# Optimization experiments

Hardware: AMD Instinct MI355X
Metric: run time of the kernel (lower is better)

Reference implementation:

```python
import jax, jax.numpy as jnp
import numpy as np

N_NODES = 100000
N_EDGES = 1600000
N_GRAPHS = 1000
IN_C = 64
HID = 64
OUT_C = 1
L = 3


def setup_inputs() -> dict:
    key = jax.random.key(0)
    ks = jax.random.split(key, 12)
    x = jax.random.normal(ks[0], (N_NODES, IN_C), dtype=jnp.float32)
    edge_index = jax.random.randint(ks[1], (2, N_EDGES), 0, N_NODES, dtype=jnp.int32)
    batch = jnp.sort(jax.random.randint(ks[2], (N_NODES,), 0, N_GRAPHS, dtype=jnp.int32))
    s = 1.0 / np.sqrt(HID)
    # GraphConv params (all layers 64->64): lin_rel (W,b) applied to aggregated
    # neighbors, lin_root (W, no bias) applied to self features.
    Wrel = jax.random.uniform(ks[3], (L, HID, HID), jnp.float32, -s, s)
    brel = jax.random.uniform(ks[4], (L, HID), jnp.float32, -s, s)
    Wroot = jax.random.uniform(ks[5], (L, HID, HID), jnp.float32, -s, s)
    W1 = jax.random.uniform(ks[6], (HID, 64), jnp.float32, -s, s)
    b1 = jax.random.uniform(ks[7], (64,), jnp.float32, -s, s)
    W2 = jax.random.uniform(ks[8], (64, 32), jnp.float32, -1/8, 1/8)
    b2 = jax.random.uniform(ks[9], (32,), jnp.float32, -1/8, 1/8)
    W3 = jax.random.uniform(ks[10], (32, OUT_C), jnp.float32, -1/np.sqrt(32), 1/np.sqrt(32))
    b3 = jax.random.uniform(ks[11], (OUT_C,), jnp.float32, -1/np.sqrt(32), 1/np.sqrt(32))
    return {"x": x, "edge_index": edge_index, "batch": batch,
            "Wrel": Wrel, "brel": brel, "Wroot": Wroot,
            "W1": W1, "b1": b1, "W2": W2, "b2": b2, "W3": W3, "b3": b3}


def reference(x, edge_index, batch, Wrel, brel, Wroot, W1, b1, W2, b2, W3, b3):
    src, dst = edge_index[0], edge_index[1]
    n = x.shape[0]
    x_add = jnp.zeros((N_GRAPHS, HID), dtype=x.dtype)
    for i in range(L):
        # GraphConv: gather source features, sum-scatter to targets
        agg = jax.ops.segment_sum(x[src], dst, num_segments=n)  # [N, C]
        x = agg @ Wrel[i] + brel[i] + x @ Wroot[i]
        x = jax.nn.relu(x)
        # global_add_pool per layer, accumulated
        x_add = x_add + jax.ops.segment_sum(x, batch, num_segments=N_GRAPHS)
    h = jax.nn.relu(x_add @ W1 + b1)
    h = jax.nn.relu(h @ W2 + b2)
    return h @ W3 + b3  # [N_GRAPHS, OUT_C]
```

## Files before the change

kernel.cpp:

```cpp
#include <hip/hip_runtime.h>
#include <hip/hip_bf16.h>

#define HID 64
#define BN 192
#define MAXB 1024

typedef short  bf16x8 __attribute__((ext_vector_type(8)));
typedef float  f32x4  __attribute__((ext_vector_type(4)));

__device__ inline float bf2f(unsigned int u16) {
    union { unsigned int i; float f; } v; v.i = u16 << 16; return v.f;
}
__device__ inline unsigned short f2bf(float f) {
    union { float f; unsigned int i; } v; v.f = f;
    unsigned int u = v.i;
    u += 0x7FFFu + ((u >> 16) & 1u);
    return (unsigned short)(u >> 16);
}

__global__ __launch_bounds__(1024) void bucket_hist(
        const int* __restrict__ dst, int* __restrict__ cnt, int E, int nb) {
    __shared__ int h[MAXB];
    for (int i = threadIdx.x; i < nb; i += 1024) h[i] = 0;
    __syncthreads();
    int base = blockIdx.x * 16384;
    for (int i = 0; i < 16; ++i) {
        int e = base + i * 1024 + threadIdx.x;
        if (e < E) atomicAdd(&h[dst[e] / BN], 1);
    }
    __syncthreads();
    for (int i = threadIdx.x; i < nb; i += 1024)
        if (h[i]) atomicAdd(&cnt[i], h[i]);
}

__global__ void bucket_scan(const int* __restrict__ cnt, int* __restrict__ base,
                            int* __restrict__ cursor, int nb, int total) {
    int lane = threadIdx.x;
    int running = 0;
    int nch = (nb + 63) / 64;
    for (int c = 0; c < nch; ++c) {
        int i = c * 64 + lane;
        int v = (i < nb) ? cnt[i] : 0;
        int s = v;
        for (int d = 1; d < 64; d <<= 1) {
            int t = __shfl_up(s, d);
            if (lane >= d) s += t;
        }
        if (i < nb) {
            int ex = running + s - v;
            base[i] = ex;
            cursor[i * 16] = ex;
        }
        running += __shfl(s, 63);
    }
    if (lane == 0) base[nb] = total;
}

__global__ __launch_bounds__(1024) void bucket_scatter(
        const int* __restrict__ src, const int* __restrict__ dst,
        int* __restrict__ cursor, unsigned int* __restrict__ rec, int E, int nb) {
    __shared__ int h[MAXB];
    __shared__ int gb[MAXB];
    __shared__ int lc[MAXB];
    for (int i = threadIdx.x; i < nb; i += 1024) { h[i] = 0; lc[i] = 0; }
    __syncthreads();
    int base = blockIdx.x * 16384;
    for (int i = 0; i < 16; ++i) {
        int e = base + i * 1024 + threadIdx.x;
        if (e < E) atomicAdd(&h[dst[e] / BN], 1);
    }
    __syncthreads();
    for (int i = threadIdx.x; i < nb; i += 1024) {
        int c = h[i];
        if (c) gb[i] = atomicAdd(&cursor[i * 16], c);
    }
    __syncthreads();
    for (int i = 0; i < 16; ++i) {
        int e = base + i * 1024 + threadIdx.x;
        if (e < E) {
            int d = dst[e];
            int b = d / BN;
            int lp = atomicAdd(&lc[b], 1);
            rec[gb[b] + lp] = ((unsigned int)src[e] << 8) | (unsigned int)(d - b * BN);
        }
    }
}

__global__ __launch_bounds__(256) void bucket_to_csr(
        const unsigned int* __restrict__ rec, const int* __restrict__ bbase,
        int* __restrict__ col, int* __restrict__ rowp, int N, int nb) {
    __shared__ int tmp[256];
    __shared__ int cur[256];
    int b = blockIdx.x;
    int n0 = b * BN;
    int nNodes = min(BN, N - n0);
    int tid = threadIdx.x;
    int e0 = bbase[b], e1 = bbase[b + 1];
    tmp[tid] = 0;
    __syncthreads();
    for (int e = e0 + tid; e < e1; e += 256)
        atomicAdd(&tmp[rec[e] & 255u], 1);
    __syncthreads();
    int my = tmp[tid];
    for (int offd = 1; offd < 256; offd <<= 1) {
        int t = (tid >= offd) ? tmp[tid - offd] : 0;
        __syncthreads();
        tmp[tid] += t;
        __syncthreads();
    }
    int ex = tmp[tid] - my;
    cur[tid] = ex;
    if (tid < nNodes) rowp[n0 + tid] = e0 + ex;
    if (b == nb - 1 && tid == 0) rowp[N] = e1;
    __syncthreads();
    for (int e = e0 + tid; e < e1; e += 256) {
        unsigned int r = rec[e];
        int p = atomicAdd(&cur[r & 255u], 1);
        col[e0 + p] = (int)(r >> 8);
    }
}

__global__ __launch_bounds__(256) void prep_all(
        const float* __restrict__ x0, unsigned int* __restrict__ xb,
        const float* __restrict__ Wrel, const float* __restrict__ Wroot,
        unsigned short* __restrict__ Wt,
        const int* __restrict__ batch, int* __restrict__ bstart,
        int* __restrict__ bcnt, float* __restrict__ x_add,
        int N, int G, int nl, int NB) {
    int i = blockIdx.x * 256 + threadIdx.x;
    if (i < N * 16) {
        float4 v = reinterpret_cast<const float4*>(x0)[i];
        xb[i * 2]     = ((unsigned int)f2bf(v.y) << 16) | f2bf(v.x);
        xb[i * 2 + 1] = ((unsigned int)f2bf(v.w) << 16) | f2bf(v.z);
    }
    if (i < nl * 64 * 128) {
        int k = i & 127, c = (i >> 7) & 63, l = i >> 13;
        float v = (k < 64) ? Wrel[(size_t)l * 4096 + k * 64 + c]
                           : Wroot[(size_t)l * 4096 + (k - 64) * 64 + c];
        Wt[i] = f2bf(v);
    }
    if (i < N) {
        int b = batch[i];
        int prev = (i == 0) ? -1 : batch[i - 1];
        for (int g = prev + 1; g <= b; ++g) bstart[g] = i;
        if (i == N - 1)
            for (int g = b + 1; g <= G; ++g) bstart[g] = N;
    }
    if (i < NB) bcnt[i] = 0;
    if (i < G * 64) x_add[i] = 0.f;
}

__global__ __launch_bounds__(256) void layer_fused(
        const int* __restrict__ rowp, const int* __restrict__ col,
        const unsigned int* __restrict__ xb,
        unsigned short* __restrict__ yout,
        const unsigned short* __restrict__ Wt,
        const float* __restrict__ brel, int n) {
    __shared__ unsigned int aggL[16][36];
    int n0 = blockIdx.x * 16;
    int tid = threadIdx.x;
    int lane = tid & 63;
    int wv = tid >> 6;
    int half = lane >> 5, ch = lane & 31;

#pragma unroll
    for (int s = 0; s < 2; ++s) {
        int node = n0 + wv * 4 + half * 2 + s;
        if (node < n) {
            int e0 = rowp[node], e1 = rowp[node + 1];
            float ax = 0.f, ay = 0.f;
            for (int eb = e0; eb < e1; eb += 8) {
                int c[8];
#pragma unroll
                for (int j = 0; j < 8; ++j) c[j] = col[min(eb + j, e1 - 1)];
                unsigned int p[8];
#pragma unroll
                for (int j = 0; j < 8; ++j) p[j] = xb[(size_t)c[j] * 32 + ch];
#pragma unroll
                for (int j = 0; j < 8; ++j) {
                    unsigned int q = (eb + j < e1) ? p[j] : 0u;
                    ax += bf2f(q & 0xFFFFu);
                    ay += bf2f(q >> 16);
                }
            }
            aggL[node - n0][ch] = ((unsigned int)f2bf(ay) << 16) | f2bf(ax);
        } else if (node - n0 < 16) {
            aggL[node - n0][ch] = 0u;
        }
    }
    __syncthreads();

    int r = lane & 15, kb = lane >> 4;
    f32x4 acc = {};
    const unsigned short* xrow = reinterpret_cast<const unsigned short*>(xb)
                               + (size_t)min(n0 + r, n - 1) * 64 + kb * 8;
    const unsigned short* wrow = Wt + (size_t)(wv * 16 + r) * 128 + kb * 8;
#pragma unroll
    for (int ks = 0; ks < 4; ++ks) {
        bf16x8 a;
        if (ks < 2) {
            a = *reinterpret_cast<const bf16x8*>(
                    reinterpret_cast<const unsigned short*>(&aggL[r][0])
                    + ks * 32 + kb * 8);
        } else {
            a = *reinterpret_cast<const bf16x8*>(xrow + (ks - 2) * 32);
        }
        bf16x8 b = *reinterpret_cast<const bf16x8*>(wrow + ks * 32);
        acc = __builtin_amdgcn_mfma_f32_16x16x32_bf16(a, b, acc, 0, 0, 0);
    }
    int c = wv * 16 + r;
    float bias = brel[c];
#pragma unroll
    for (int reg = 0; reg < 4; ++reg) {
        int node = n0 + kb * 4 + reg;
        if (node < n) {
            float v = acc[reg] + bias;
            yout[(size_t)node * 64 + c] = f2bf(fmaxf(v, 0.f));
        }
    }
}

__global__ __launch_bounds__(256) void pool_bf16(
        const unsigned int* __restrict__ y,
        const int* __restrict__ bstart, float* __restrict__ x_add, int ngraph) {
    int g = blockIdx.x;
    if (g >= ngraph) return;
    int lane = threadIdx.x & 63, w = threadIdx.x >> 6;
    int h = lane >> 5, ch = lane & 31;
    __shared__ float2 part[4][32];
    int s0 = bstart[g], s1 = bstart[g + 1];
    float ax = 0.f, ay = 0.f;
    for (int nd = s0 + w * 2 + h; nd < s1; nd += 8) {
        unsigned int p = y[(size_t)nd * 32 + ch];
        ax += bf2f(p & 0xFFFFu);
        ay += bf2f(p >> 16);
    }
    ax += __shfl(ax, lane ^ 32);
    ay += __shfl(ay, lane ^ 32);
    if (h == 0) part[w][ch] = make_float2(ax, ay);
    __syncthreads();
    if (threadIdx.x < 32) {
        float2 s = part[0][threadIdx.x];
        s.x += part[1][threadIdx.x].x + part[2][threadIdx.x].x + part[3][threadIdx.x].x;
        s.y += part[1][threadIdx.x].y + part[2][threadIdx.x].y + part[3][threadIdx.x].y;
        float2* xa = reinterpret_cast<float2*>(x_add + (size_t)g * 64);
        float2 cur = xa[threadIdx.x];
        xa[threadIdx.x] = make_float2(cur.x + s.x, cur.y + s.y);
    }
}

__global__ __launch_bounds__(64) void mlp_kernel(
        const float* __restrict__ x_add,
        const float* __restrict__ W1, const float* __restrict__ b1,
        const float* __restrict__ W2, const float* __restrict__ b2,
        const float* __restrict__ W3, const float* __restrict__ b3,
        float* __restrict__ out, int ngraph) {
    int g = blockIdx.x;
    if (g >= ngraph) return;
    int lane = threadIdx.x;
    __shared__ float h1s[64];
    __shared__ float h2s[32];
    const float* xa = x_add + (size_t)g * HID;
    float s = b1[lane];
#pragma unroll
    for (int k = 0; k < 64; ++k) s += xa[k] * W1[k * 64 + lane];
    h1s[lane] = fmaxf(s, 0.f);
    __syncthreads();
    if (lane < 32) {
        float s2 = b2[lane];
#pragma unroll
        for (int k = 0; k < 64; ++k) s2 += h1s[k] * W2[k * 32 + lane];
        h2s[lane] = fmaxf(s2, 0.f);
    }
    __syncthreads();
    if (lane == 0) {
        float o = b3[0];
        for (int k = 0; k < 32; ++k) o += h2s[k] * W3[k];
        out[g] = o;
    }
}

extern "C" void kernel_launch(void* const* d_in, const int* in_sizes, int n_in,
                              void* d_out, int out_size, void* d_ws, size_t ws_size,
                              hipStream_t stream) {
    const float* x0    = (const float*)d_in[0];
    const int*   ei    = (const int*)d_in[1];
    const int*   batch = (const int*)d_in[2];
    const float* Wrel  = (const float*)d_in[3];
    const float* brel  = (const float*)d_in[4];
    const float* Wroot = (const float*)d_in[5];
    const float* W1    = (const float*)d_in[6];
    const float* b1    = (const float*)d_in[7];
    const float* W2    = (const float*)d_in[8];
    const float* b2    = (const float*)d_in[9];
    const float* W3    = (const float*)d_in[10];
    const float* b3    = (const float*)d_in[11];
    float* out = (float*)d_out;

    const int N = in_sizes[0] / HID;
    const int E = in_sizes[1] / 2;
    const int G = out_size;
    const int L = in_sizes[3] / (HID * HID);
    const int NB = (N + BN - 1) / BN;

    const int* src = ei;
    const int* dst = ei + E;

    char* w = (char*)d_ws;
    size_t off = 0;
    auto alloc = [&](size_t bytes) {
        void* p = w + off;
        off += (bytes + 255) & ~(size_t)255;
        return p;
    };
    unsigned short* xb0   = (unsigned short*)alloc((size_t)N * HID * 2);
    unsigned short* xbA   = (unsigned short*)alloc((size_t)N * HID * 2);
    unsigned short* xbB   = (unsigned short*)alloc((size_t)N * HID * 2);
    unsigned short* Wt    = (unsigned short*)alloc((size_t)L * 64 * 128 * 2);
    unsigned int*   recs  = (unsigned int*)alloc((size_t)E * 4);
    int*   col    = (int*)alloc((size_t)E * 4);
    int*   rowp   = (int*)alloc((size_t)(N + 1) * 4);
    float* x_add  = (float*)alloc((size_t)G * HID * 4);
    int*   bcnt   = (int*)alloc((size_t)NB * 4);
    int*   bbase  = (int*)alloc((size_t)(NB + 1) * 4);
    int*   bcur   = (int*)alloc((size_t)NB * 16 * 4);
    int*   bstart = (int*)alloc((size_t)(G + 1) * 4);
    (void)ws_size;

    const int TB = 256;

    prep_all<<<(N * 16 + TB - 1) / TB, TB, 0, stream>>>(
            x0, (unsigned int*)xb0, Wrel, Wroot, Wt,
            batch, bstart, bcnt, x_add, N, G, L, NB);

    int sortBlocks = (E + 16383) / 16384;
    bucket_hist<<<sortBlocks, 1024, 0, stream>>>(dst, bcnt, E, NB);
    bucket_scan<<<1, 64, 0, stream>>>(bcnt, bbase, bcur, NB, E);
    bucket_scatter<<<sortBlocks, 1024, 0, stream>>>(src, dst, bcur, recs, E, NB);
    bucket_to_csr<<<NB, TB, 0, stream>>>(recs, bbase, col, rowp, N, NB);

    int tileBlocks = (N + 15) / 16;
    for (int i = 0; i < L; ++i) {
        const unsigned short* xin = (i == 0) ? xb0 : ((i == 1) ? xbA : xbB);
        unsigned short* xout = (i == 1) ? xbB : xbA;
        layer_fused<<<tileBlocks, TB, 0, stream>>>(rowp, col,
                (const unsigned int*)xin, xout,
                Wt + (size_t)i * 64 * 128, brel + (size_t)i * HID, N);
        pool_bf16<<<G, TB, 0, stream>>>((const unsigned int*)xout, bstart, x_add, G);
    }

    mlp_kernel<<<G, 64, 0, stream>>>(x_add, W1, b1, W2, b2, W3, b3, out, G);
}
```

Measured before the change: 228.4 us.

## Reuse per-block histograms in scatter and fold pooling into layer and MLP kernels

```diff
diff --git a/kernel.cpp b/kernel.cpp
--- a/kernel.cpp
+++ b/kernel.cpp
@@ -19,7 +19,8 @@
 }
 
 __global__ __launch_bounds__(1024) void bucket_hist(
-        const int* __restrict__ dst, int* __restrict__ cnt, int E, int nb) {
+        const int* __restrict__ dst, int* __restrict__ cnt,
+        int* __restrict__ gHist, int E, int nb) {
     __shared__ int h[MAXB];
     for (int i = threadIdx.x; i < nb; i += 1024) h[i] = 0;
     __syncthreads();
@@ -29,8 +30,12 @@
         if (e < E) atomicAdd(&h[dst[e] / BN], 1);
     }
     __syncthreads();
-    for (int i = threadIdx.x; i < nb; i += 1024)
-        if (h[i]) atomicAdd(&cnt[i], h[i]);
+    int* gh = gHist + (size_t)blockIdx.x * nb;
+    for (int i = threadIdx.x; i < nb; i += 1024) {
+        int c = h[i];
+        gh[i] = c;
+        if (c) atomicAdd(&cnt[i], c);
+    }
 }
 
 __global__ void bucket_scan(const int* __restrict__ cnt, int* __restrict__ base,
@@ -58,23 +63,18 @@
 
 __global__ __launch_bounds__(1024) void bucket_scatter(
         const int* __restrict__ src, const int* __restrict__ dst,
+        const int* __restrict__ gHist,
         int* __restrict__ cursor, unsigned int* __restrict__ rec, int E, int nb) {
-    __shared__ int h[MAXB];
     __shared__ int gb[MAXB];
     __shared__ int lc[MAXB];
-    for (int i = threadIdx.x; i < nb; i += 1024) { h[i] = 0; lc[i] = 0; }
+    for (int i = threadIdx.x; i < nb; i += 1024) lc[i] = 0;
+    const int* gh = gHist + (size_t)blockIdx.x * nb;
+    for (int i = threadIdx.x; i < nb; i += 1024) {
+        int c = gh[i];
+        if (c) gb[i] = atomicAdd(&cursor[i * 16], c);
+    }
     __syncthreads();
     int base = blockIdx.x * 16384;
-    for (int i = 0; i < 16; ++i) {
-        int e = base + i * 1024 + threadIdx.x;
-        if (e < E) atomicAdd(&h[dst[e] / BN], 1);
-    }
-    __syncthreads();
-    for (int i = threadIdx.x; i < nb; i += 1024) {
-        int c = h[i];
-        if (c) gb[i] = atomicAdd(&cursor[i * 16], c);
-    }
-    __syncthreads();
     for (int i = 0; i < 16; ++i) {
         int e = base + i * 1024 + threadIdx.x;
         if (e < E) {
@@ -155,10 +155,41 @@
         const unsigned int* __restrict__ xb,
         unsigned short* __restrict__ yout,
         const unsigned short* __restrict__ Wt,
-        const float* __restrict__ brel, int n) {
+        const float* __restrict__ brel,
+        const unsigned int* __restrict__ poolY,
+        const int* __restrict__ bstart, float* __restrict__ x_add,
+        int n, int nTiles, int G) {
+    int tid = threadIdx.x;
+    if (blockIdx.x >= nTiles) {
+        int g = blockIdx.x - nTiles;
+        if (g >= G) return;
+        int lane = tid & 63, w = tid >> 6;
+        int h = lane >> 5, ch = lane & 31;
+        __shared__ float2 part[4][32];
+        int s0 = bstart[g], s1 = bstart[g + 1];
+        float ax = 0.f, ay = 0.f;
+        for (int nd = s0 + w * 2 + h; nd < s1; nd += 8) {
+            unsigned int p = poolY[(size_t)nd * 32 + ch];
+            ax += bf2f(p & 0xFFFFu);
+            ay += bf2f(p >> 16);
+        }
+        ax += __shfl(ax, lane ^ 32);
+        ay += __shfl(ay, lane ^ 32);
+        if (h == 0) part[w][ch] = make_float2(ax, ay);
+        __syncthreads();
+        if (tid < 32) {
+            float2 s = part[0][tid];
+            s.x += part[1][tid].x + part[2][tid].x + part[3][tid].x;
+            s.y += part[1][tid].y + part[2][tid].y + part[3][tid].y;
+            float2* xa = reinterpret_cast<float2*>(x_add + (size_t)g * 64);
+            float2 cur = xa[tid];
+            xa[tid] = make_float2(cur.x + s.x, cur.y + s.y);
+        }
+        return;
+    }
+
     __shared__ unsigned int aggL[16][36];
     int n0 = blockIdx.x * 16;
-    int tid = threadIdx.x;
     int lane = tid & 63;
     int wv = tid >> 6;
     int half = lane >> 5, ch = lane & 31;
@@ -220,60 +251,58 @@
     }
 }
 
-__global__ __launch_bounds__(256) void pool_bf16(
-        const unsigned int* __restrict__ y,
-        const int* __restrict__ bstart, float* __restrict__ x_add, int ngraph) {
-    int g = blockIdx.x;
-    if (g >= ngraph) return;
-    int lane = threadIdx.x & 63, w = threadIdx.x >> 6;
-    int h = lane >> 5, ch = lane & 31;
-    __shared__ float2 part[4][32];
-    int s0 = bstart[g], s1 = bstart[g + 1];
-    float ax = 0.f, ay = 0.f;
-    for (int nd = s0 + w * 2 + h; nd < s1; nd += 8) {
-        unsigned int p = y[(size_t)nd * 32 + ch];
-        ax += bf2f(p & 0xFFFFu);
-        ay += bf2f(p >> 16);
-    }
-    ax += __shfl(ax, lane ^ 32);
-    ay += __shfl(ay, lane ^ 32);
-    if (h == 0) part[w][ch] = make_float2(ax, ay);
-    __syncthreads();
-    if (threadIdx.x < 32) {
-        float2 s = part[0][threadIdx.x];
-        s.x += part[1][threadIdx.x].x + part[2][threadIdx.x].x + part[3][threadIdx.x].x;
-        s.y += part[1][threadIdx.x].y + part[2][threadIdx.x].y + part[3][threadIdx.x].y;
-        float2* xa = reinterpret_cast<float2*>(x_add + (size_t)g * 64);
-        float2 cur = xa[threadIdx.x];
-        xa[threadIdx.x] = make_float2(cur.x + s.x, cur.y + s.y);
-    }
-}
-
-__global__ __launch_bounds__(64) void mlp_kernel(
-        const float* __restrict__ x_add,
+__global__ __launch_bounds__(256) void final_pool_mlp(
+        const unsigned int* __restrict__ y3,
+        const int* __restrict__ bstart, const float* __restrict__ x_add,
         const float* __restrict__ W1, const float* __restrict__ b1,
         const float* __restrict__ W2, const float* __restrict__ b2,
         const float* __restrict__ W3, const float* __restrict__ b3,
         float* __restrict__ out, int ngraph) {
     int g = blockIdx.x;
     if (g >= ngraph) return;
-    int lane = threadIdx.x;
+    int tid = threadIdx.x;
+    int lane = tid & 63, w = tid >> 6;
+    int h = lane >> 5, ch = lane & 31;
+    __shared__ float2 part[4][32];
+    __shared__ float xaL[64];
     __shared__ float h1s[64];
     __shared__ float h2s[32];
-    const float* xa = x_add + (size_t)g * HID;
-    float s = b1[lane];
-#pragma unroll
-    for (int k = 0; k < 64; ++k) s += xa[k] * W1[k * 64 + lane];
-    h1s[lane] = fmaxf(s, 0.f);
-    __syncthreads();
-    if (lane < 32) {
-        float s2 = b2[lane];
-#pragma unroll
-        for (int k = 0; k < 64; ++k) s2 += h1s[k] * W2[k * 32 + lane];
-        h2s[lane] = fmaxf(s2, 0.f);
-    }
-    __syncthreads();
-    if (lane == 0) {
+    int s0 = bstart[g], s1 = bstart[g + 1];
+    float ax = 0.f, ay = 0.f;
+    for (int nd = s0 + w * 2 + h; nd < s1; nd += 8) {
+        unsigned int p = y3[(size_t)nd * 32 + ch];
+        ax += bf2f(p & 0xFFFFu);
+        ay += bf2f(p >> 16);
+    }
+    ax += __shfl(ax, lane ^ 32);
+    ay += __shfl(ay, lane ^ 32);
+    if (h == 0) part[w][ch] = make_float2(ax, ay);
+    __syncthreads();
+    if (tid < 32) {
+        float2 s = part[0][tid];
+        s.x += part[1][tid].x + part[2][tid].x + part[3][tid].x;
+        s.y += part[1][tid].y + part[2][tid].y + part[3][tid].y;
+        const float2* xa = reinterpret_cast<const float2*>(x_add + (size_t)g * 64);
+        float2 cur = xa[tid];
+        xaL[tid * 2]     = cur.x + s.x;
+        xaL[tid * 2 + 1] = cur.y + s.y;
+    }
+    __syncthreads();
+    if (tid < 64) {
+        float s = b1[tid];
+#pragma unroll
+        for (int k = 0; k < 64; ++k) s += xaL[k] * W1[k * 64 + tid];
+        h1s[tid] = fmaxf(s, 0.f);
+    }
+    __syncthreads();
+    if (tid < 32) {
+        float s2 = b2[tid];
+#pragma unroll
+        for (int k = 0; k < 64; ++k) s2 += h1s[k] * W2[k * 32 + tid];
+        h2s[tid] = fmaxf(s2, 0.f);
+    }
+    __syncthreads();
+    if (tid == 0) {
         float o = b3[0];
         for (int k = 0; k < 32; ++k) o += h2s[k] * W3[k];
         out[g] = o;
@@ -313,6 +342,8 @@
         off += (bytes + 255) & ~(size_t)255;
         return p;
     };
+    int sortBlocks = (E + 16383) / 16384;
+
     unsigned short* xb0   = (unsigned short*)alloc((size_t)N * HID * 2);
     unsigned short* xbA   = (unsigned short*)alloc((size_t)N * HID * 2);
     unsigned short* xbB   = (unsigned short*)alloc((size_t)N * HID * 2);
@@ -325,6 +356,7 @@
     int*   bbase  = (int*)alloc((size_t)(NB + 1) * 4);
     int*   bcur   = (int*)alloc((size_t)NB * 16 * 4);
     int*   bstart = (int*)alloc((size_t)(G + 1) * 4);
+    int*   gHist  = (int*)alloc((size_t)sortBlocks * NB * 4);
     (void)ws_size;
 
     const int TB = 256;
@@ -333,21 +365,23 @@
             x0, (unsigned int*)xb0, Wrel, Wroot, Wt,
             batch, bstart, bcnt, x_add, N, G, L, NB);
 
-    int sortBlocks = (E + 16383) / 16384;
-    bucket_hist<<<sortBlocks, 1024, 0, stream>>>(dst, bcnt, E, NB);
+    bucket_hist<<<sortBlocks, 1024, 0, stream>>>(dst, bcnt, gHist, E, NB);
     bucket_scan<<<1, 64, 0, stream>>>(bcnt, bbase, bcur, NB, E);
-    bucket_scatter<<<sortBlocks, 1024, 0, stream>>>(src, dst, bcur, recs, E, NB);
+    bucket_scatter<<<sortBlocks, 1024, 0, stream>>>(src, dst, gHist, bcur, recs, E, NB);
     bucket_to_csr<<<NB, TB, 0, stream>>>(recs, bbase, col, rowp, N, NB);
 
-    int tileBlocks = (N + 15) / 16;
+    int nTiles = (N + 15) / 16;
     for (int i = 0; i < L; ++i) {
         const unsigned short* xin = (i == 0) ? xb0 : ((i == 1) ? xbA : xbB);
         unsigned short* xout = (i == 1) ? xbB : xbA;
-        layer_fused<<<tileBlocks, TB, 0, stream>>>(rowp, col,
+        const unsigned int* poolY = (i == 0) ? nullptr : (const unsigned int*)xin;
+        int grid = (i == 0) ? nTiles : (nTiles + G);
+        layer_fused<<<grid, TB, 0, stream>>>(rowp, col,
                 (const unsigned int*)xin, xout,
-                Wt + (size_t)i * 64 * 128, brel + (size_t)i * HID, N);
-        pool_bf16<<<G, TB, 0, stream>>>((const unsigned int*)xout, bstart, x_add, G);
-    }
-
-    mlp_kernel<<<G, 64, 0, stream>>>(x_add, W1, b1, W2, b2, W3, b3, out, G);
-}
+                Wt + (size_t)i * 64 * 128, brel + (size_t)i * HID,
+                poolY, bstart, x_add, N, nTiles, G);
+    }
+
+    final_pool_mlp<<<G, TB, 0, stream>>>((const unsigned int*)xbA, bstart, x_add,
+            W1, b1, W2, b2, W3, b3, out, G);
+}
```

Result: faster. 211.5 us (-7.4%).
